# Performance work log

Hardware: AMD Instinct MI355X
Metric: run time of the kernel (lower is better)

The kernel has to match this reference:

```python
import jax, jax.numpy as jnp
import numpy as np
from jax import lax

SHARP = 1.0
NEG_INF = -1e30


def setup_inputs() -> dict:
    key = jax.random.key(0)
    k1, k2, k3 = jax.random.split(key, 3)
    nt, nb, nf = 2000, 256, 5
    ns = 500
    x = jax.random.normal(k1, (nt, nb, nf), dtype=jnp.float32)
    seqs = jax.random.randint(k2, (nb, ns), 0, 4, dtype=jnp.int32)       # base moves index features 0..3
    seqlens = jax.random.randint(k3, (nb,), 0, ns + 1, dtype=jnp.int32)  # index into fwd of width ns+1
    return {"x": x, "seqs": seqs, "seqlens": seqlens}


def reference(x, seqs, seqlens):
    nt, nb, nf = x.shape
    ns = seqs.shape[1]
    # fwd[:, 0] = 0, rest = -inf
    fwd0 = jnp.full((nb, ns + 1), NEG_INF, dtype=x.dtype).at[:, 0].set(0.0)

    def step(fwd, xt):
        xt = xt * SHARP                                      # (nb, 5)
        score = xt[:, 4][:, None] + fwd                      # stay transition, (nb, ns+1)
        move = jnp.take_along_axis(xt, seqs, axis=1) + fwd[:, :-1]  # move transition, (nb, ns)
        score = score.at[:, 1:].set(jnp.logaddexp(move, score[:, 1:]))
        return score, None

    fwd, _ = lax.scan(step, fwd0, x)
    return -jnp.take_along_axis(fwd, seqlens[:, None].astype(jnp.int32), axis=1) / (nt * SHARP)
```

## Files before the change

kernel.cpp:

```cpp
#include <hip/hip_runtime.h>

#define NT 2000
#define NB 256
#define NF 5
#define NS 500
#define LOG0   (-1e30f)
#define LOG2E  1.44269504088896340736f
#define LN2F   0.69314718055994530942f
#define RSTRIDE 2024

__device__ __forceinline__ float wave_shr1(float v) {
    return __int_as_float(
        __builtin_amdgcn_mov_dpp(__float_as_int(v), 0x138, 0xf, 0xf, true));
}

__global__ __launch_bounds__(256) void ctc_fwd_kernel(
    const float* __restrict__ x,
    const int*   __restrict__ seqs,
    const int*   __restrict__ seqlens,
    float*       __restrict__ out)
{
    __shared__ __align__(16) float wtabT[4 * RSTRIDE];
    __shared__ float Gbuf[576];
    __shared__ float red[256];

    const int b    = blockIdx.x;
    const int tid  = threadIdx.x;
    const int wave = tid >> 6;
    const int lane = tid & 63;

    float csum = 0.f;
    for (int t = tid; t < NT; t += 256) {
        const float* xp = x + (size_t)t * (NB * NF) + b * NF;
        const float x4 = xp[4];
        wtabT[0 * RSTRIDE + t] = __builtin_amdgcn_exp2f((xp[0] - x4) * LOG2E);
        wtabT[1 * RSTRIDE + t] = __builtin_amdgcn_exp2f((xp[1] - x4) * LOG2E);
        wtabT[2 * RSTRIDE + t] = __builtin_amdgcn_exp2f((xp[2] - x4) * LOG2E);
        wtabT[3 * RSTRIDE + t] = __builtin_amdgcn_exp2f((xp[3] - x4) * LOG2E);
        csum += x4;
    }
    for (int i = tid; i < 576; i += 256) Gbuf[i] = LOG0;
    red[tid] = csum;
    __syncthreads();
    for (int off = 128; off > 0; off >>= 1) {
        if (tid < off) red[tid] += red[tid + off];
        __syncthreads();
    }

    const int wbase = wave * 128 - 64;
    const int rel0 = 3 * lane;
    const int s0 = wbase + rel0, s1 = s0 + 1, s2 = s0 + 2;

    const int i0 = (s0 >= 1 && s0 <= NS) ? seqs[b * NS + s0 - 1] : 0;
    const int i1 = (s1 >= 1 && s1 <= NS) ? seqs[b * NS + s1 - 1] : 0;
    const int i2 = (s2 >= 1 && s2 <= NS) ? seqs[b * NS + s2 - 1] : 0;
    const float* wrow0 = &wtabT[i0 * RSTRIDE];
    const float* wrow1 = &wtabT[i1 * RSTRIDE];
    const float* wrow2 = &wtabT[i2 * RSTRIDE];

    float p0 = (s0 == 0) ? 1.f : 0.f;
    float p1 = (s1 == 0) ? 1.f : 0.f;
    float p2 = (s2 == 0) ? 1.f : 0.f;
    float Lw  = 0.f;
    float adj = 1.f;

#define STEP(W0A, W1, W2) do {                \
        const float sh = wave_shr1(p2);       \
        p2 = fmaf(p1, (W2), p2);              \
        p1 = fmaf(p0, (W1), p1);              \
        p0 = fmaf(sh, (W0A), p0);             \
    } while (0)

    for (int c = 0; c < 125; ++c) {
        if (c > 0) {
            if ((c & 3) == 0) {
                __syncthreads();
                if (rel0     >= 64) Gbuf[64 + s0] = (p0 > 0.f) ? __builtin_amdgcn_logf(p0) + Lw : LOG0;
                if (rel0 + 1 >= 64) Gbuf[64 + s1] = (p1 > 0.f) ? __builtin_amdgcn_logf(p1) + Lw : LOG0;
                if (rel0 + 2 >= 64) Gbuf[64 + s2] = (p2 > 0.f) ? __builtin_amdgcn_logf(p2) + Lw : LOG0;
                __syncthreads();
                const float g0 = Gbuf[64 + s0];
                const float g1 = Gbuf[64 + s1];
                const float g2 = Gbuf[64 + s2];
                const float ref = fmaxf(fmaxf(g0, g1), g2);
                const bool alive = (ref > 0.5f * LOG0);
                const unsigned long long mk = __ballot(alive);
                float fb = 0.f;
                if (mk) {
                    const int lastlive = 63 - __builtin_clzll(mk);
                    fb = __int_as_float(
                        __builtin_amdgcn_readlane(__float_as_int(ref), lastlive));
                }
                Lw = alive ? ref : fb;
                p0 = __builtin_amdgcn_exp2f(g0 - Lw);
                p1 = __builtin_amdgcn_exp2f(g1 - Lw);
                p2 = __builtin_amdgcn_exp2f(g2 - Lw);
            } else {
                const float m = fmaxf(fmaxf(p0, p1), p2);
                if (m > 0.f) {
                    const float inv = __builtin_amdgcn_rcpf(m);
                    Lw += __builtin_amdgcn_logf(m);
                    p0 *= inv; p1 *= inv; p2 *= inv;
                }
            }
            const float Lwp = wave_shr1(Lw);
            adj = __builtin_amdgcn_exp2f(fminf(Lwp - Lw, 100.f));
        }
        const int tb = c << 4;
        #pragma unroll
        for (int q = 0; q < 4; ++q) {
            const float4 wa = *reinterpret_cast<const float4*>(wrow0 + tb + 4 * q);
            const float4 wb = *reinterpret_cast<const float4*>(wrow1 + tb + 4 * q);
            const float4 wc = *reinterpret_cast<const float4*>(wrow2 + tb + 4 * q);
            STEP(wa.x * adj, wb.x, wc.x);
            STEP(wa.y * adj, wb.y, wc.y);
            STEP(wa.z * adj, wb.z, wc.z);
            STEP(wa.w * adj, wb.w, wc.w);
        }
    }
#undef STEP

    __syncthreads();
    if (rel0     >= 64) Gbuf[64 + s0] = (p0 > 0.f) ? __builtin_amdgcn_logf(p0) + Lw : LOG0;
    if (rel0 + 1 >= 64) Gbuf[64 + s1] = (p1 > 0.f) ? __builtin_amdgcn_logf(p1) + Lw : LOG0;
    if (rel0 + 2 >= 64) Gbuf[64 + s2] = (p2 > 0.f) ? __builtin_amdgcn_logf(p2) + Lw : LOG0;
    __syncthreads();
    if (tid == 0) {
        const int sl = seqlens[b];
        out[b] = -(Gbuf[64 + sl] * LN2F + red[0]) * (1.0f / (float)NT);
    }
}

extern "C" void kernel_launch(void* const* d_in, const int* in_sizes, int n_in,
                              void* d_out, int out_size, void* d_ws, size_t ws_size,
                              hipStream_t stream) {
    const float* x       = (const float*)d_in[0];
    const int*   seqs    = (const int*)d_in[1];
    const int*   seqlens = (const int*)d_in[2];
    float*       out     = (float*)d_out;

    ctc_fwd_kernel<<<dim3(NB), dim3(256), 0, stream>>>(x, seqs, seqlens, out);
}
```

Before: 130.8 us.

## Double-buffer LDS weight loads across chunks and remap block-to-batch order

Adds register double-buffering so the next chunk's 48 weight values are loaded from LDS while the current chunk's serial recurrence runs, hiding LDS latency behind the DPP/FMA chain. It also sets launch_bounds to one block per CU, which frees more registers for the extra buffers, and permutes the block-to-batch mapping so the strided global reads of x are spread differently across the grid. The cost is much higher register pressure, with a risk of spills, plus code duplication from the unrolled even/odd branches.

```diff
diff --git a/kernel.cpp b/kernel.cpp
--- a/kernel.cpp
+++ b/kernel.cpp
@@ -14,7 +14,7 @@
         __builtin_amdgcn_mov_dpp(__float_as_int(v), 0x138, 0xf, 0xf, true));
 }
 
-__global__ __launch_bounds__(256) void ctc_fwd_kernel(
+__global__ __launch_bounds__(256, 1) void ctc_fwd_kernel(
     const float* __restrict__ x,
     const int*   __restrict__ seqs,
     const int*   __restrict__ seqlens,
@@ -24,7 +24,7 @@
     __shared__ float Gbuf[576];
     __shared__ float red[256];
 
-    const int b    = blockIdx.x;
+    const int b    = ((blockIdx.x & 7) << 5) | (blockIdx.x >> 3);
     const int tid  = threadIdx.x;
     const int wave = tid >> 6;
     const int lane = tid & 63;
@@ -71,6 +71,40 @@
         p0 = fmaf(sh, (W0A), p0);             \
     } while (0)
 
+    float4 Xa0, Xa1, Xa2, Xa3, Xb0, Xb1, Xb2, Xb3, Xc0, Xc1, Xc2, Xc3;
+    float4 Ya0, Ya1, Ya2, Ya3, Yb0, Yb1, Yb2, Yb3, Yc0, Yc1, Yc2, Yc3;
+
+#define PRELOAD(P, TB) do {                                            \
+        const int _tb = (TB);                                          \
+        P##a0 = *reinterpret_cast<const float4*>(wrow0 + _tb);         \
+        P##a1 = *reinterpret_cast<const float4*>(wrow0 + _tb + 4);     \
+        P##a2 = *reinterpret_cast<const float4*>(wrow0 + _tb + 8);     \
+        P##a3 = *reinterpret_cast<const float4*>(wrow0 + _tb + 12);    \
+        P##b0 = *reinterpret_cast<const float4*>(wrow1 + _tb);         \
+        P##b1 = *reinterpret_cast<const float4*>(wrow1 + _tb + 4);     \
+        P##b2 = *reinterpret_cast<const float4*>(wrow1 + _tb + 8);     \
+        P##b3 = *reinterpret_cast<const float4*>(wrow1 + _tb + 12);    \
+        P##c0 = *reinterpret_cast<const float4*>(wrow2 + _tb);         \
+        P##c1 = *reinterpret_cast<const float4*>(wrow2 + _tb + 4);     \
+        P##c2 = *reinterpret_cast<const float4*>(wrow2 + _tb + 8);     \
+        P##c3 = *reinterpret_cast<const float4*>(wrow2 + _tb + 12);    \
+    } while (0)
+
+#define QSTEP(WA, WB, WC) do {                \
+        STEP(WA.x * adj, WB.x, WC.x);         \
+        STEP(WA.y * adj, WB.y, WC.y);         \
+        STEP(WA.z * adj, WB.z, WC.z);         \
+        STEP(WA.w * adj, WB.w, WC.w);         \
+    } while (0)
+
+#define COMPUTE(P) do {                       \
+        QSTEP(P##a0, P##b0, P##c0);           \
+        QSTEP(P##a1, P##b1, P##c1);           \
+        QSTEP(P##a2, P##b2, P##c2);           \
+        QSTEP(P##a3, P##b3, P##c3);           \
+    } while (0)
+
+    PRELOAD(X, 0);
     for (int c = 0; c < 125; ++c) {
         if (c > 0) {
             if ((c & 3) == 0) {
@@ -106,18 +140,17 @@
             const float Lwp = wave_shr1(Lw);
             adj = __builtin_amdgcn_exp2f(fminf(Lwp - Lw, 100.f));
         }
-        const int tb = c << 4;
-        #pragma unroll
-        for (int q = 0; q < 4; ++q) {
-            const float4 wa = *reinterpret_cast<const float4*>(wrow0 + tb + 4 * q);
-            const float4 wb = *reinterpret_cast<const float4*>(wrow1 + tb + 4 * q);
-            const float4 wc = *reinterpret_cast<const float4*>(wrow2 + tb + 4 * q);
-            STEP(wa.x * adj, wb.x, wc.x);
-            STEP(wa.y * adj, wb.y, wc.y);
-            STEP(wa.z * adj, wb.z, wc.z);
-            STEP(wa.w * adj, wb.w, wc.w);
+        if ((c & 1) == 0) {
+            if (c < 124) PRELOAD(Y, (c + 1) << 4);
+            COMPUTE(X);
+        } else {
+            if (c < 124) PRELOAD(X, (c + 1) << 4);
+            COMPUTE(Y);
         }
     }
+#undef COMPUTE
+#undef QSTEP
+#undef PRELOAD
 #undef STEP
 
     __syncthreads();
```

New measurement: 136.0 us. 4.0% more time.

## Split each sequence over eight waves with two states per lane

Applied to the files above, without the earlier changes.

Each block now runs 512 threads (8 waves), and each lane holds 2 states instead of 3. This shortens the serial FMA/DPP chain per timestep, at the cost of more barriers across more waves and more overlap lanes. Each wave now owns 64 new states, so the 64-lane overlap region makes half its lanes redundant. Block indices are also remapped so neighbouring blocks handle batch items spread across the batch, presumably to spread them over XCDs or memory channels.

```diff
diff --git a/kernel.cpp b/kernel.cpp
--- a/kernel.cpp
+++ b/kernel.cpp
@@ -14,7 +14,7 @@
         __builtin_amdgcn_mov_dpp(__float_as_int(v), 0x138, 0xf, 0xf, true));
 }
 
-__global__ __launch_bounds__(256) void ctc_fwd_kernel(
+__global__ __launch_bounds__(512, 1) void ctc_fwd_kernel(
     const float* __restrict__ x,
     const int*   __restrict__ seqs,
     const int*   __restrict__ seqlens,
@@ -22,15 +22,15 @@
 {
     __shared__ __align__(16) float wtabT[4 * RSTRIDE];
     __shared__ float Gbuf[576];
-    __shared__ float red[256];
+    __shared__ float red[512];
 
-    const int b    = blockIdx.x;
+    const int b    = ((blockIdx.x & 7) << 5) | (blockIdx.x >> 3);
     const int tid  = threadIdx.x;
     const int wave = tid >> 6;
     const int lane = tid & 63;
 
     float csum = 0.f;
-    for (int t = tid; t < NT; t += 256) {
+    for (int t = tid; t < NT; t += 512) {
         const float* xp = x + (size_t)t * (NB * NF) + b * NF;
         const float x4 = xp[4];
         wtabT[0 * RSTRIDE + t] = __builtin_amdgcn_exp2f((xp[0] - x4) * LOG2E);
@@ -39,50 +39,54 @@
         wtabT[3 * RSTRIDE + t] = __builtin_amdgcn_exp2f((xp[3] - x4) * LOG2E);
         csum += x4;
     }
-    for (int i = tid; i < 576; i += 256) Gbuf[i] = LOG0;
+    for (int i = tid; i < 576; i += 512) Gbuf[i] = LOG0;
     red[tid] = csum;
     __syncthreads();
-    for (int off = 128; off > 0; off >>= 1) {
+    for (int off = 256; off > 0; off >>= 1) {
         if (tid < off) red[tid] += red[tid + off];
         __syncthreads();
     }
 
-    const int wbase = wave * 128 - 64;
-    const int rel0 = 3 * lane;
-    const int s0 = wbase + rel0, s1 = s0 + 1, s2 = s0 + 2;
+    const int wbase = wave * 64 - 64;
+    const int rel0 = 2 * lane;
+    const int s0 = wbase + rel0, s1 = s0 + 1;
+    const bool owned = (rel0 >= 64);
 
     const int i0 = (s0 >= 1 && s0 <= NS) ? seqs[b * NS + s0 - 1] : 0;
     const int i1 = (s1 >= 1 && s1 <= NS) ? seqs[b * NS + s1 - 1] : 0;
-    const int i2 = (s2 >= 1 && s2 <= NS) ? seqs[b * NS + s2 - 1] : 0;
     const float* wrow0 = &wtabT[i0 * RSTRIDE];
     const float* wrow1 = &wtabT[i1 * RSTRIDE];
-    const float* wrow2 = &wtabT[i2 * RSTRIDE];
 
     float p0 = (s0 == 0) ? 1.f : 0.f;
     float p1 = (s1 == 0) ? 1.f : 0.f;
-    float p2 = (s2 == 0) ? 1.f : 0.f;
     float Lw  = 0.f;
     float adj = 1.f;
 
-#define STEP(W0A, W1, W2) do {                \
-        const float sh = wave_shr1(p2);       \
-        p2 = fmaf(p1, (W2), p2);              \
+#define STEP(W0A, W1) do {                    \
+        const float sh = wave_shr1(p1);       \
         p1 = fmaf(p0, (W1), p1);              \
         p0 = fmaf(sh, (W0A), p0);             \
+    } while (0)
+
+#define QSTEP(WA, WB) do {                    \
+        STEP(WA.x * adj, WB.x);               \
+        STEP(WA.y * adj, WB.y);               \
+        STEP(WA.z * adj, WB.z);               \
+        STEP(WA.w * adj, WB.w);               \
     } while (0)
 
     for (int c = 0; c < 125; ++c) {
         if (c > 0) {
             if ((c & 3) == 0) {
                 __syncthreads();
-                if (rel0     >= 64) Gbuf[64 + s0] = (p0 > 0.f) ? __builtin_amdgcn_logf(p0) + Lw : LOG0;
-                if (rel0 + 1 >= 64) Gbuf[64 + s1] = (p1 > 0.f) ? __builtin_amdgcn_logf(p1) + Lw : LOG0;
-                if (rel0 + 2 >= 64) Gbuf[64 + s2] = (p2 > 0.f) ? __builtin_amdgcn_logf(p2) + Lw : LOG0;
+                if (owned) {
+                    Gbuf[64 + s0] = (p0 > 0.f) ? __builtin_amdgcn_logf(p0) + Lw : LOG0;
+                    Gbuf[64 + s1] = (p1 > 0.f) ? __builtin_amdgcn_logf(p1) + Lw : LOG0;
+                }
                 __syncthreads();
                 const float g0 = Gbuf[64 + s0];
                 const float g1 = Gbuf[64 + s1];
-                const float g2 = Gbuf[64 + s2];
-                const float ref = fmaxf(fmaxf(g0, g1), g2);
+                const float ref = fmaxf(g0, g1);
                 const bool alive = (ref > 0.5f * LOG0);
                 const unsigned long long mk = __ballot(alive);
                 float fb = 0.f;
@@ -94,36 +98,41 @@
                 Lw = alive ? ref : fb;
                 p0 = __builtin_amdgcn_exp2f(g0 - Lw);
                 p1 = __builtin_amdgcn_exp2f(g1 - Lw);
-                p2 = __builtin_amdgcn_exp2f(g2 - Lw);
             } else {
-                const float m = fmaxf(fmaxf(p0, p1), p2);
+                const float m = fmaxf(p0, p1);
                 if (m > 0.f) {
                     const float inv = __builtin_amdgcn_rcpf(m);
                     Lw += __builtin_amdgcn_logf(m);
-                    p0 *= inv; p1 *= inv; p2 *= inv;
+                    p0 *= inv; p1 *= inv;
                 }
             }
             const float Lwp = wave_shr1(Lw);
             adj = __builtin_amdgcn_exp2f(fminf(Lwp - Lw, 100.f));
         }
         const int tb = c << 4;
-        #pragma unroll
-        for (int q = 0; q < 4; ++q) {
-            const float4 wa = *reinterpret_cast<const float4*>(wrow0 + tb + 4 * q);
-            const float4 wb = *reinterpret_cast<const float4*>(wrow1 + tb + 4 * q);
-            const float4 wc = *reinterpret_cast<const float4*>(wrow2 + tb + 4 * q);
-            STEP(wa.x * adj, wb.x, wc.x);
-            STEP(wa.y * adj, wb.y, wc.y);
-            STEP(wa.z * adj, wb.z, wc.z);
-            STEP(wa.w * adj, wb.w, wc.w);
+        {
+            const float4 a0 = *reinterpret_cast<const float4*>(wrow0 + tb);
+            const float4 a1 = *reinterpret_cast<const float4*>(wrow0 + tb + 4);
+            const float4 a2 = *reinterpret_cast<const float4*>(wrow0 + tb + 8);
+            const float4 a3 = *reinterpret_cast<const float4*>(wrow0 + tb + 12);
+            const float4 b0 = *reinterpret_cast<const float4*>(wrow1 + tb);
+            const float4 b1 = *reinterpret_cast<const float4*>(wrow1 + tb + 4);
+            const float4 b2 = *reinterpret_cast<const float4*>(wrow1 + tb + 8);
+            const float4 b3 = *reinterpret_cast<const float4*>(wrow1 + tb + 12);
+            QSTEP(a0, b0);
+            QSTEP(a1, b1);
+            QSTEP(a2, b2);
+            QSTEP(a3, b3);
         }
     }
+#undef QSTEP
 #undef STEP
 
     __syncthreads();
-    if (rel0     >= 64) Gbuf[64 + s0] = (p0 > 0.f) ? __builtin_amdgcn_logf(p0) + Lw : LOG0;
-    if (rel0 + 1 >= 64) Gbuf[64 + s1] = (p1 > 0.f) ? __builtin_amdgcn_logf(p1) + Lw : LOG0;
-    if (rel0 + 2 >= 64) Gbuf[64 + s2] = (p2 > 0.f) ? __builtin_amdgcn_logf(p2) + Lw : LOG0;
+    if (owned) {
+        Gbuf[64 + s0] = (p0 > 0.f) ? __builtin_amdgcn_logf(p0) + Lw : LOG0;
+        Gbuf[64 + s1] = (p1 > 0.f) ? __builtin_amdgcn_logf(p1) + Lw : LOG0;
+    }
     __syncthreads();
     if (tid == 0) {
         const int sl = seqlens[b];
@@ -139,5 +148,5 @@
     const int*   seqlens = (const int*)d_in[2];
     float*       out     = (float*)d_out;
 
-    ctc_fwd_kernel<<<dim3(NB), dim3(256), 0, stream>>>(x, seqs, seqlens, out);
+    ctc_fwd_kernel<<<dim3(NB), dim3(512), 0, stream>>>(x, seqs, seqlens, out);
 }
```

After: 119.6 us. 1.09x faster.
